# Optimization experiments

Measured on AMD Instinct MI355X. Metric: run time of the kernel, lower is better.

Reference implementation:

```python
import jax, jax.numpy as jnp
import numpy as np

V, D, B, L = 10000, 300, 64, 128
CF = 5.0   # concentrator_factor
EPS = 1e-8  # torch cosine_similarity eps


def setup_inputs() -> dict:
    key = jax.random.key(0)
    ks = jax.random.split(key, 7)
    concepts_list = jax.random.randint(ks[0], (B, L), 0, V)
    concepts_length = jax.random.randint(ks[1], (B,), 0, L + 1)
    embed_w = jax.random.normal(ks[2], (V, D), jnp.float32)
    concept_w = jax.random.normal(ks[3], (V, D), jnp.float32)
    em = jax.random.uniform(ks[4], (V, V), jnp.float32)
    # init_params normalization: row-max minus col-min, per row
    rng = (em.max(axis=1) - em.min(axis=0))[:, None]
    edge_matrix = em / (rng + (rng == 0).astype(em.dtype))
    affectiveness = jax.random.uniform(ks[5], (V,), jnp.float32)
    lam = jax.random.uniform(ks[6], (V,), jnp.float32)
    return {
        "concepts_list": concepts_list,
        "concepts_length": concepts_length,
        "embed_w": embed_w,
        "concept_w": concept_w,
        "edge_matrix": edge_matrix,
        "affectiveness": affectiveness,
        "lam": lam,
    }


def reference(concepts_list, concepts_length, embed_w, concept_w, edge_matrix, affectiveness, lam):
    b, l = concepts_list.shape
    mask = (jnp.arange(l)[None, :] < concepts_length[:, None]).astype(embed_w.dtype)  # [B,L]
    denom = jnp.maximum(concepts_length, 1).astype(embed_w.dtype)[:, None]            # [B,1]

    # context representation: ragged per-sample mean, then mean over batch
    ce = embed_w[concepts_list]                                  # [B,L,D]
    per_sample = (ce * mask[:, :, None]).sum(axis=1) / denom     # [B,D] (zeros for empty)
    context = per_sample.mean(axis=0)                            # [D]

    # |cosine similarity| of context vs every concept embedding row
    cn = jnp.linalg.norm(context)
    rn = jnp.linalg.norm(concept_w, axis=1)                      # [V]
    cos = jnp.abs((concept_w @ context) / jnp.maximum(cn * rn, EPS))  # [V]

    em = edge_matrix[concepts_list]                              # [B,L,V]
    rel = em * cos
    aff = (em > 0).astype(em.dtype) * affectiveness
    weights = lam * rel + (1.0 - lam) * aff                      # [B,L,V]
    probs = jax.nn.softmax(weights * CF, axis=2)                 # [B,L,V]
    ce2 = jnp.einsum('blv,vd->bld', probs, concept_w)            # [B,L,D]

    out = (ce2 * mask[:, :, None]).sum(axis=1) / denom           # [B,D] (zeros for empty)
    return out
```

## Files before the change

kernel.cpp:

```cpp
#include <hip/hip_runtime.h>
#include <math.h>

#define NV 10000
#define ND 300
#define NB 64
#define NL 128
#define CFv 5.0f
#define EPSV 1e-8f

#define WS_CTX   0
#define WS_CN    300
#define WS_CNT   301
#define WS_A     320
#define WS_B     10320
#define WS_ROWS  20320
#define WS_S     28512
#define WS_WTG   36704

#define KR    128
#define WTGLD 10112
#define NKR   79
#define GMG   6
#define NTI   19
#define MT    32
#define SOB   16

typedef __attribute__((ext_vector_type(8))) __bf16 bf16x8;
typedef __attribute__((ext_vector_type(4))) float f32x4;

static __device__ __forceinline__ unsigned short f2bf(float x) {
  union { float f; unsigned u; } v; v.f = x;
  unsigned r = v.u + 0x7fffu + ((v.u >> 16) & 1u);
  return (unsigned short)(r >> 16);
}

__global__ __launch_bounds__(256) void k_init(float* __restrict__ out, float* __restrict__ wsf) {
  int g = blockIdx.x * 256 + threadIdx.x;
  if (g < NB * ND) out[g] = 0.f;
  if (g < 302) wsf[g] = 0.f;
}

#define CSL 4
__global__ __launch_bounds__(320) void k_context(const int* __restrict__ clist,
                                                 const int* __restrict__ clen,
                                                 const float* __restrict__ embed,
                                                 float* __restrict__ wsf) {
  __shared__ int kl[NL];
  int b = blockIdx.x / CSL, sl = blockIdx.x % CSL;
  int d = threadIdx.x;
  int len = clen[b];
  if (d < NL) kl[d] = clist[b * NL + d];
  __syncthreads();
  if (d >= ND) return;
  float acc = 0.f;
  for (int l = sl; l < len; l += CSL)
    acc += embed[(long)kl[l] * ND + d];
  float dn = (float)(len > 0 ? len : 1);
  atomicAdd(&wsf[WS_CTX + d], acc * (1.0f / NB) / dn);
}

__global__ __launch_bounds__(320) void k_cn(float* __restrict__ wsf) {
  __shared__ float red[5];
  int t = threadIdx.x;
  float x = (t < ND) ? wsf[WS_CTX + t] : 0.f;
  float s = x * x;
  #pragma unroll
  for (int o = 32; o; o >>= 1) s += __shfl_xor(s, o);
  if ((t & 63) == 0) red[t >> 6] = s;
  __syncthreads();
  if (t == 0) {
    float tot = 0.f;
    #pragma unroll
    for (int i = 0; i < 5; ++i) tot += red[i];
    wsf[WS_CN] = sqrtf(tot);
  }
}

__global__ __launch_bounds__(256) void k_cos(const float* __restrict__ cw,
                                             const float* __restrict__ lam,
                                             const float* __restrict__ aff,
                                             float* __restrict__ wsf) {
  int wid = threadIdx.x >> 6, lane = threadIdx.x & 63;
  int v = blockIdx.x * 4 + wid;
  const float* row = cw + (long)v * ND;
  float dot = 0.f, rn2 = 0.f;
  for (int d = lane; d < ND; d += 64) {
    float w = row[d], c = wsf[WS_CTX + d];
    dot += w * c;
    rn2 += w * w;
  }
  #pragma unroll
  for (int o = 32; o; o >>= 1) { dot += __shfl_xor(dot, o); rn2 += __shfl_xor(rn2, o); }
  if (lane == 0) {
    float cn = wsf[WS_CN];
    float cosv = fabsf(dot) / fmaxf(cn * sqrtf(rn2), EPSV);
    float lv = lam[v];
    wsf[WS_A + v] = CFv * lv * cosv;
    wsf[WS_B + v] = CFv * (1.f - lv) * aff[v];
  }
}

__global__ __launch_bounds__(256) void k_wt(const float* __restrict__ cw, float* __restrict__ wsf) {
  __shared__ unsigned short T[304][68];
  int tid = threadIdx.x;
  int v0 = blockIdx.x * 64;
  for (int q = tid; q < 304 * 68 / 2; q += 256) ((unsigned*)&T[0][0])[q] = 0u;
  __syncthreads();
  const float4* cw4 = (const float4*)cw;
  for (int q = tid; q < 64 * 75; q += 256) {
    int r = q / 75, p = q - r * 75;
    int v = v0 + r;
    if (v < NV) {
      float4 w = cw4[(long)v * 75 + p];
      T[4 * p + 0][r] = f2bf(w.x);
      T[4 * p + 1][r] = f2bf(w.y);
      T[4 * p + 2][r] = f2bf(w.z);
      T[4 * p + 3][r] = f2bf(w.w);
    }
  }
  __syncthreads();
  unsigned short* wtg = (unsigned short*)(wsf + WS_WTG);
  for (int q = tid; q < 304 * 16; q += 256) {
    int n = q >> 4, rp = q & 15;
    *(ushort4*)&wtg[(long)n * WTGLD + v0 + 4 * rp] = *(const ushort4*)&T[n][4 * rp];
  }
}

__global__ __launch_bounds__(256) void k_compact(const int* __restrict__ clen, int* __restrict__ wsi) {
  __shared__ int cum[NB + 1];
  int tid = threadIdx.x;
  if (tid == 0) {
    int c = 0;
    for (int b = 0; b < NB; ++b) {
      cum[b] = c;
      int ln = clen[b]; if (ln < 0) ln = 0; if (ln > NL) ln = NL;
      c += ln;
    }
    cum[NB] = c;
    wsi[WS_CNT] = c;
  }
  __syncthreads();
  for (int t = tid; t < NB * NL; t += 256) {
    int b = t >> 7, l = t & 127;
    int len = cum[b + 1] - cum[b];
    if (l < len) wsi[WS_ROWS + cum[b] + l] = t;
  }
}

__global__ __launch_bounds__(256) void k_srow(const int* __restrict__ clist,
                                              const float* __restrict__ edge,
                                              float* __restrict__ wsf) {
  const int* wsi = (const int*)wsf;
  int wid = threadIdx.x >> 6, lane = threadIdx.x & 63;
  int pos = blockIdx.x * 4 + wid;
  int count = wsi[WS_CNT];
  if (pos >= count) return;
  int row = wsi[WS_ROWS + pos];
  const float4* e4 = (const float4*)(edge + (long)clist[row] * NV);
  const float4* A4 = (const float4*)(wsf + WS_A);
  const float4* B4 = (const float4*)(wsf + WS_B);
  float sp = 0.f;
  for (int v = lane; v < NV / 4; v += 64) {
    float4 em = e4[v], a = A4[v], b = B4[v];
    sp += __expf(fmaf(a.x, em.x, (em.x > 0.f) ? b.x : 0.f));
    sp += __expf(fmaf(a.y, em.y, (em.y > 0.f) ? b.y : 0.f));
    sp += __expf(fmaf(a.z, em.z, (em.z > 0.f) ? b.z : 0.f));
    sp += __expf(fmaf(a.w, em.w, (em.w > 0.f) ? b.w : 0.f));
  }
  #pragma unroll
  for (int o = 32; o; o >>= 1) sp += __shfl_xor(sp, o);
  if (lane == 0) wsf[WS_S + pos] = sp;
}

__global__ __launch_bounds__(512, 4) void k_main(const int* __restrict__ clist,
                                                 const int* __restrict__ clen,
                                                 const float* __restrict__ edge,
                                                 const float* __restrict__ wsf,
                                                 float* __restrict__ out) {
  __shared__ unsigned short ebuf[2][MT * KR];
  __shared__ float cls[2][KR];
  __shared__ float sout[SOB][304];
  __shared__ int   rb_s[2][MT];
  __shared__ float scl_s[2][MT];

  const int* wsi = (const int*)wsf;
  const unsigned short* wtg = (const unsigned short*)(wsf + WS_WTG);
  int tid = threadIdx.x;
  int count = wsi[WS_CNT];
  int Mtiles = (count + MT - 1) / MT;
  int kr = blockIdx.x / GMG, g = blockIdx.x % GMG;
  int v0 = kr * KR;
  int klen = NV - v0; if (klen > KR) klen = KR;
  int nch = (klen + 31) >> 5;
  int tpg = (Mtiles + GMG - 1) / GMG;
  int mt0 = g * tpg;
  int mt1 = min(mt0 + tpg, Mtiles);

  int b0 = 0;
  {
    int r0c = mt0 * MT;
    if (r0c < count) b0 = wsi[WS_ROWS + r0c] >> 7;
  }

  for (int q = tid; q < 2 * KR; q += 512) {
    int a = q >> 7, k = q & (KR - 1);
    float val = 0.f;
    if (v0 + k < NV) val = wsf[(a ? WS_B : WS_A) + v0 + k];
    cls[a][k] = val;
  }
  for (int q = tid; q < SOB * 304; q += 512) ((float*)sout)[q] = 0.f;

  int wv = tid >> 6, lane = tid & 63;
  int q4 = lane >> 4, l15 = lane & 15;
  int nt0 = (wv * NTI) >> 3, nt1 = ((wv + 1) * NTI) >> 3;

  bf16x8 bfrag[3][4] = {};
  #pragma unroll
  for (int j = 0; j < 3; ++j)
    #pragma unroll
    for (int c5 = 0; c5 < 4; ++c5)
      if (nt0 + j < nt1 && c5 < nch) {
        int n = (nt0 + j) * 16 + l15;
        bfrag[j][c5] = *(const bf16x8*)(const void*)&wtg[(long)n * WTGLD + v0 + c5 * 32 + q4 * 8];
      }

  __syncthreads();

  float4 eld[2];
  int    vld[2];
  int    m_row; float m_scl;

  auto stage_load = [&](int mtx, bool valid) {
    int r0 = mtx * MT;
    #pragma unroll
    for (int j = 0; j < 2; ++j) {
      vld[j] = 0;
      int q = tid + j * 512;
      int rm = q >> 5, k = (q & 31) * 4;
      int pos = r0 + rm;
      if (valid && pos < count && k < klen) {
        int rowid = wsi[WS_ROWS + pos];
        eld[j] = *(const float4*)(edge + (long)clist[rowid] * NV + v0 + k);
        vld[j] = 1;
      }
    }
    m_row = -1; m_scl = 0.f;
    if (tid < MT) {
      int pos = r0 + tid;
      if (valid && pos < count) {
        int rowid = wsi[WS_ROWS + pos];
        float S = wsf[WS_S + pos];
        int ln = clen[rowid >> 7];
        m_row = rowid;
        m_scl = 1.0f / (S * (float)(ln > 0 ? ln : 1));
      }
    }
  };

  auto stage_write = [&](int nb) {
    char* eb = (char*)&ebuf[nb][0];
    #pragma unroll
    for (int j = 0; j < 2; ++j) {
      int q = tid + j * 512;
      int rm = q >> 5, k = (q & 31) * 4;
      ushort4 ev = make_ushort4(0, 0, 0, 0);
      if (vld[j]) {
        float4 a = *(const float4*)&cls[0][k];
        float4 b = *(const float4*)&cls[1][k];
        float4 em = eld[j];
        ev.x = f2bf(__expf(fmaf(a.x, em.x, (em.x > 0.f) ? b.x : 0.f)));
        ev.y = f2bf(__expf(fmaf(a.y, em.y, (em.y > 0.f) ? b.y : 0.f)));
        ev.z = f2bf(__expf(fmaf(a.z, em.z, (em.z > 0.f) ? b.z : 0.f)));
        ev.w = f2bf(__expf(fmaf(a.w, em.w, (em.w > 0.f) ? b.w : 0.f)));
      }
      int off = (rm << 8) + (k << 1);
      off ^= (rm & 7) << 4;
      *(ushort4*)(eb + off) = ev;
    }
    if (tid < MT) { rb_s[nb][tid] = m_row; scl_s[nb][tid] = m_scl; }
  };

  int curb = -1;
  float rs0 = 0.f, rs1 = 0.f, rs2 = 0.f;
  auto emit = [&](int b, float s0, float s1, float s2) {
    if (b < 0) return;
    #pragma unroll
    for (int j = 0; j < 3; ++j) {
      if (nt0 + j < nt1) {
        int n = (nt0 + j) * 16 + l15;
        if (n < ND) {
          float v = (j == 0) ? s0 : (j == 1) ? s1 : s2;
          int rel = b - b0;
          if (rel >= 0 && rel < SOB) atomicAdd(&sout[rel][n], v);
          else atomicAdd(&out[b * ND + n], v);
        }
      }
    }
  };

  if (mt0 < mt1) {
    stage_load(mt0, true);
    stage_write(0);
    __syncthreads();

    int cb = 0;
    for (int mt = mt0; mt < mt1; ++mt) {
      stage_load(mt + 1, mt + 1 < mt1);

      f32x4 acc[2][3] = {};
      const char* eb = (const char*)&ebuf[cb][0];
      #pragma unroll
      for (int c5 = 0; c5 < 4; ++c5) {
        if (c5 < nch) {
          int kb2 = (c5 * 32 + q4 * 8) << 1;
          int off0 = ((l15 << 8) + kb2) ^ ((l15 & 7) << 4);
          int off1 = (((16 + l15) << 8) + kb2) ^ ((l15 & 7) << 4);
          bf16x8 a0 = *(const bf16x8*)(const void*)(eb + off0);
          bf16x8 a1 = *(const bf16x8*)(const void*)(eb + off1);
          #pragma unroll
          for (int j = 0; j < 3; ++j) {
            if (nt0 + j < nt1) {
              acc[0][j] = __builtin_amdgcn_mfma_f32_16x16x32_bf16(a0, bfrag[j][c5], acc[0][j], 0, 0, 0);
              acc[1][j] = __builtin_amdgcn_mfma_f32_16x16x32_bf16(a1, bfrag[j][c5], acc[1][j], 0, 0, 0);
            }
          }
        }
      }

      stage_write(cb ^ 1);

      #pragma unroll
      for (int ms = 0; ms < 2; ++ms)
        #pragma unroll
        for (int r = 0; r < 4; ++r) {
          int m = ms * 16 + q4 * 4 + r;
          int row = rb_s[cb][m];
          if (row >= 0) {
            int b = row >> 7;
            float sc = scl_s[cb][m];
            if (b != curb) {
              emit(curb, rs0, rs1, rs2);
              curb = b; rs0 = rs1 = rs2 = 0.f;
            }
            rs0 += acc[ms][0][r] * sc;
            rs1 += acc[ms][1][r] * sc;
            rs2 += acc[ms][2][r] * sc;
          }
        }

      __syncthreads();
      cb ^= 1;
    }
    emit(curb, rs0, rs1, rs2);
  }
  __syncthreads();

  for (int q = tid; q < SOB * 304; q += 512) {
    int s = q / 304, n = q - s * 304;
    float v = sout[s][n];
    if (n < ND && v != 0.f) {
      int b = b0 + s;
      if (b < NB) atomicAdd(&out[b * ND + n], v);
    }
  }
}

extern "C" void kernel_launch(void* const* d_in, const int* in_sizes, int n_in,
                              void* d_out, int out_size, void* d_ws, size_t ws_size,
                              hipStream_t stream) {
  const int*   clist = (const int*)d_in[0];
  const int*   clen  = (const int*)d_in[1];
  const float* embed = (const float*)d_in[2];
  const float* cw    = (const float*)d_in[3];
  const float* edge  = (const float*)d_in[4];
  const float* aff   = (const float*)d_in[5];
  const float* lam   = (const float*)d_in[6];
  float* out = (float*)d_out;
  float* wsf = (float*)d_ws;
  int*   wsi = (int*)d_ws;

  hipLaunchKernelGGL(k_init,    dim3(77),          dim3(256), 0, stream, out, wsf);
  hipLaunchKernelGGL(k_context, dim3(NB * CSL),    dim3(320), 0, stream, clist, clen, embed, wsf);
  hipLaunchKernelGGL(k_cn,      dim3(1),           dim3(320), 0, stream, wsf);
  hipLaunchKernelGGL(k_cos,     dim3(NV / 4),      dim3(256), 0, stream, cw, lam, aff, wsf);
  hipLaunchKernelGGL(k_wt,      dim3(WTGLD / 64),  dim3(256), 0, stream, cw, wsf);
  hipLaunchKernelGGL(k_compact, dim3(1),           dim3(256), 0, stream, clen, wsi);
  hipLaunchKernelGGL(k_srow,    dim3(NB * NL / 4), dim3(256), 0, stream, clist, edge, wsf);
  hipLaunchKernelGGL(k_main,    dim3(NKR * GMG),   dim3(512), 0, stream,
                     clist, clen, edge, wsf, out);
}
```

Baseline: 180.7 us.

## Deepen main-loop prefetch to two tiles and parallelize row compaction with wave scan

The main loop now holds two register sets of staged edge loads, so global loads for tile mt+2 are issued while tile mt is computed, giving a two-tile prefetch distance instead of one. The loop is manually unrolled by two with named A/B buffers, which avoids dynamic indexing into register arrays. Separately, the compaction kernel replaces its serial prefix sum with a 64-lane shuffle scan and spreads the row scatter across 32 blocks. Keeping extra in-flight registers raises register pressure and could reduce occupancy.

```diff
diff --git a/kernel.cpp b/kernel.cpp
--- a/kernel.cpp
+++ b/kernel.cpp
@@ -129,22 +129,23 @@
 __global__ __launch_bounds__(256) void k_compact(const int* __restrict__ clen, int* __restrict__ wsi) {
   __shared__ int cum[NB + 1];
   int tid = threadIdx.x;
-  if (tid == 0) {
-    int c = 0;
-    for (int b = 0; b < NB; ++b) {
-      cum[b] = c;
-      int ln = clen[b]; if (ln < 0) ln = 0; if (ln > NL) ln = NL;
-      c += ln;
-    }
-    cum[NB] = c;
-    wsi[WS_CNT] = c;
-  }
-  __syncthreads();
-  for (int t = tid; t < NB * NL; t += 256) {
-    int b = t >> 7, l = t & 127;
-    int len = cum[b + 1] - cum[b];
-    if (l < len) wsi[WS_ROWS + cum[b] + l] = t;
-  }
+  if (tid < 64) {
+    int ln = clen[tid]; ln = min(max(ln, 0), NL);
+    int s = ln;
+    #pragma unroll
+    for (int o = 1; o < 64; o <<= 1) {
+      int t = __shfl_up(s, o);
+      if (tid >= o) s += t;
+    }
+    cum[tid + 1] = s;
+    if (tid == 0) cum[0] = 0;
+    if (tid == 63) wsi[WS_CNT] = s;
+  }
+  __syncthreads();
+  int t = blockIdx.x * 256 + tid;
+  int b = t >> 7, l = t & 127;
+  int len = cum[b + 1] - cum[b];
+  if (l < len) wsi[WS_ROWS + cum[b] + l] = t;
 }
 
 __global__ __launch_bounds__(256) void k_srow(const int* __restrict__ clist,
@@ -226,11 +227,13 @@
 
   __syncthreads();
 
-  float4 eld[2];
-  int    vld[2];
-  int    m_row; float m_scl;
-
-  auto stage_load = [&](int mtx, bool valid) {
+  float4 eldA[2], eldB[2];
+  int    vldA[2], vldB[2];
+  int    m_rowA = -1, m_rowB = -1;
+  float  m_sclA = 0.f, m_sclB = 0.f;
+
+  auto stage_load = [&](int mtx, bool valid, float4 (&eld)[2], int (&vld)[2],
+                        int& m_row, float& m_scl) {
     int r0 = mtx * MT;
     #pragma unroll
     for (int j = 0; j < 2; ++j) {
@@ -257,7 +260,8 @@
     }
   };
 
-  auto stage_write = [&](int nb) {
+  auto stage_write = [&](int nb, const float4 (&eld)[2], const int (&vld)[2],
+                         int m_row, float m_scl) {
     char* eb = (char*)&ebuf[nb][0];
     #pragma unroll
     for (int j = 0; j < 2; ++j) {
@@ -280,6 +284,27 @@
     if (tid < MT) { rb_s[nb][tid] = m_row; scl_s[nb][tid] = m_scl; }
   };
 
+  auto do_mfma = [&](int nb, f32x4 (&acc)[2][3]) {
+    const char* eb = (const char*)&ebuf[nb][0];
+    #pragma unroll
+    for (int c5 = 0; c5 < 4; ++c5) {
+      if (c5 < nch) {
+        int kb2 = (c5 * 32 + q4 * 8) << 1;
+        int off0 = ((l15 << 8) + kb2) ^ ((l15 & 7) << 4);
+        int off1 = (((16 + l15) << 8) + kb2) ^ ((l15 & 7) << 4);
+        bf16x8 a0 = *(const bf16x8*)(const void*)(eb + off0);
+        bf16x8 a1 = *(const bf16x8*)(const void*)(eb + off1);
+        #pragma unroll
+        for (int j = 0; j < 3; ++j) {
+          if (nt0 + j < nt1) {
+            acc[0][j] = __builtin_amdgcn_mfma_f32_16x16x32_bf16(a0, bfrag[j][c5], acc[0][j], 0, 0, 0);
+            acc[1][j] = __builtin_amdgcn_mfma_f32_16x16x32_bf16(a1, bfrag[j][c5], acc[1][j], 0, 0, 0);
+          }
+        }
+      }
+    }
+  };
+
   int curb = -1;
   float rs0 = 0.f, rs1 = 0.f, rs2 = 0.f;
   auto emit = [&](int b, float s0, float s1, float s2) {
@@ -298,58 +323,48 @@
     }
   };
 
+  auto fold = [&](const f32x4 (&acc)[2][3], int nb) {
+    #pragma unroll
+    for (int ms = 0; ms < 2; ++ms)
+      #pragma unroll
+      for (int r = 0; r < 4; ++r) {
+        int m = ms * 16 + q4 * 4 + r;
+        int row = rb_s[nb][m];
+        if (row >= 0) {
+          int b = row >> 7;
+          float sc = scl_s[nb][m];
+          if (b != curb) {
+            emit(curb, rs0, rs1, rs2);
+            curb = b; rs0 = rs1 = rs2 = 0.f;
+          }
+          rs0 += acc[ms][0][r] * sc;
+          rs1 += acc[ms][1][r] * sc;
+          rs2 += acc[ms][2][r] * sc;
+        }
+      }
+  };
+
   if (mt0 < mt1) {
-    stage_load(mt0, true);
-    stage_write(0);
+    stage_load(mt0, true, eldA, vldA, m_rowA, m_sclA);
+    stage_write(0, eldA, vldA, m_rowA, m_sclA);
+    stage_load(mt0 + 1, mt0 + 1 < mt1, eldB, vldB, m_rowB, m_sclB);
     __syncthreads();
 
-    int cb = 0;
-    for (int mt = mt0; mt < mt1; ++mt) {
-      stage_load(mt + 1, mt + 1 < mt1);
-
-      f32x4 acc[2][3] = {};
-      const char* eb = (const char*)&ebuf[cb][0];
-      #pragma unroll
-      for (int c5 = 0; c5 < 4; ++c5) {
-        if (c5 < nch) {
-          int kb2 = (c5 * 32 + q4 * 8) << 1;
-          int off0 = ((l15 << 8) + kb2) ^ ((l15 & 7) << 4);
-          int off1 = (((16 + l15) << 8) + kb2) ^ ((l15 & 7) << 4);
-          bf16x8 a0 = *(const bf16x8*)(const void*)(eb + off0);
-          bf16x8 a1 = *(const bf16x8*)(const void*)(eb + off1);
-          #pragma unroll
-          for (int j = 0; j < 3; ++j) {
-            if (nt0 + j < nt1) {
-              acc[0][j] = __builtin_amdgcn_mfma_f32_16x16x32_bf16(a0, bfrag[j][c5], acc[0][j], 0, 0, 0);
-              acc[1][j] = __builtin_amdgcn_mfma_f32_16x16x32_bf16(a1, bfrag[j][c5], acc[1][j], 0, 0, 0);
-            }
-          }
-        }
-      }
-
-      stage_write(cb ^ 1);
-
-      #pragma unroll
-      for (int ms = 0; ms < 2; ++ms)
-        #pragma unroll
-        for (int r = 0; r < 4; ++r) {
-          int m = ms * 16 + q4 * 4 + r;
-          int row = rb_s[cb][m];
-          if (row >= 0) {
-            int b = row >> 7;
-            float sc = scl_s[cb][m];
-            if (b != curb) {
-              emit(curb, rs0, rs1, rs2);
-              curb = b; rs0 = rs1 = rs2 = 0.f;
-            }
-            rs0 += acc[ms][0][r] * sc;
-            rs1 += acc[ms][1][r] * sc;
-            rs2 += acc[ms][2][r] * sc;
-          }
-        }
-
+    for (int mt = mt0; mt < mt1; mt += 2) {
+      stage_load(mt + 2, mt + 2 < mt1, eldA, vldA, m_rowA, m_sclA);
+      f32x4 acc0[2][3] = {};
+      do_mfma(0, acc0);
+      stage_write(1, eldB, vldB, m_rowB, m_sclB);
+      fold(acc0, 0);
       __syncthreads();
-      cb ^= 1;
+      if (mt + 1 < mt1) {
+        stage_load(mt + 3, mt + 3 < mt1, eldB, vldB, m_rowB, m_sclB);
+        f32x4 acc1[2][3] = {};
+        do_mfma(1, acc1);
+        stage_write(0, eldA, vldA, m_rowA, m_sclA);
+        fold(acc1, 1);
+        __syncthreads();
+      }
     }
     emit(curb, rs0, rs1, rs2);
   }
@@ -384,7 +399,7 @@
   hipLaunchKernelGGL(k_cn,      dim3(1),           dim3(320), 0, stream, wsf);
   hipLaunchKernelGGL(k_cos,     dim3(NV / 4),      dim3(256), 0, stream, cw, lam, aff, wsf);
   hipLaunchKernelGGL(k_wt,      dim3(WTGLD / 64),  dim3(256), 0, stream, cw, wsf);
-  hipLaunchKernelGGL(k_compact, dim3(1),           dim3(256), 0, stream, clen, wsi);
+  hipLaunchKernelGGL(k_compact, dim3(32),          dim3(256), 0, stream, clen, wsi);
   hipLaunchKernelGGL(k_srow,    dim3(NB * NL / 4), dim3(256), 0, stream, clist, edge, wsf);
   hipLaunchKernelGGL(k_main,    dim3(NKR * GMG),   dim3(512), 0, stream,
                      clist, clen, edge, wsf, out);
```

Measured after the change: 394.0 us. 118% more time.

## Materialize bf16 exp-weights in row-sum pass and stream them into MFMA kernel

Applied to the files above, without the earlier changes.

The row-sum kernel now also writes the exponentiated, bf16-rounded edge weights for every compacted row into a padded workspace matrix and stores the final per-row scale. The main MFMA kernel reads these bf16 tiles directly from global memory instead of reloading fp32 edge rows, recomputing exp, and staging through double-buffered LDS. This removes duplicate exp work and the second fp32 edge read, at the cost of a large extra workspace write/read and loss of the LDS pipeline and its coalescing/swizzle.

```diff
diff --git a/kernel.cpp b/kernel.cpp
--- a/kernel.cpp
+++ b/kernel.cpp
@@ -16,14 +16,19 @@
 #define WS_ROWS  20320
 #define WS_S     28512
 #define WS_WTG   36704
+#define WS_E     1573760
 
 #define KR    128
 #define WTGLD 10112
+#define ELD   10112
+#define NV4   2500
+#define NV4P  2528
 #define NKR   79
 #define GMG   6
 #define NTI   19
 #define MT    32
 #define SOB   16
+#define TPM   1376
 
 typedef __attribute__((ext_vector_type(8))) __bf16 bf16x8;
 typedef __attribute__((ext_vector_type(4))) float f32x4;
@@ -148,43 +153,56 @@
 }
 
 __global__ __launch_bounds__(256) void k_srow(const int* __restrict__ clist,
+                                              const int* __restrict__ clen,
                                               const float* __restrict__ edge,
                                               float* __restrict__ wsf) {
   const int* wsi = (const int*)wsf;
   int wid = threadIdx.x >> 6, lane = threadIdx.x & 63;
   int pos = blockIdx.x * 4 + wid;
   int count = wsi[WS_CNT];
-  if (pos >= count) return;
+  int countR = (count + 31) & ~31;
+  if (pos >= countR) return;
+  ushort4* Erow = (ushort4*)((unsigned short*)(wsf + WS_E) + (long)pos * ELD);
+  if (pos >= count) {
+    ushort4 z = make_ushort4(0, 0, 0, 0);
+    for (int v = lane; v < NV4P; v += 64) Erow[v] = z;
+    return;
+  }
   int row = wsi[WS_ROWS + pos];
   const float4* e4 = (const float4*)(edge + (long)clist[row] * NV);
   const float4* A4 = (const float4*)(wsf + WS_A);
   const float4* B4 = (const float4*)(wsf + WS_B);
   float sp = 0.f;
-  for (int v = lane; v < NV / 4; v += 64) {
-    float4 em = e4[v], a = A4[v], b = B4[v];
-    sp += __expf(fmaf(a.x, em.x, (em.x > 0.f) ? b.x : 0.f));
-    sp += __expf(fmaf(a.y, em.y, (em.y > 0.f) ? b.y : 0.f));
-    sp += __expf(fmaf(a.z, em.z, (em.z > 0.f) ? b.z : 0.f));
-    sp += __expf(fmaf(a.w, em.w, (em.w > 0.f) ? b.w : 0.f));
+  for (int v = lane; v < NV4P; v += 64) {
+    ushort4 ev = make_ushort4(0, 0, 0, 0);
+    if (v < NV4) {
+      float4 em = e4[v], a = A4[v], b = B4[v];
+      float e0 = __expf(fmaf(a.x, em.x, (em.x > 0.f) ? b.x : 0.f));
+      float e1 = __expf(fmaf(a.y, em.y, (em.y > 0.f) ? b.y : 0.f));
+      float e2 = __expf(fmaf(a.z, em.z, (em.z > 0.f) ? b.z : 0.f));
+      float e3 = __expf(fmaf(a.w, em.w, (em.w > 0.f) ? b.w : 0.f));
+      sp += e0 + e1 + e2 + e3;
+      ev.x = f2bf(e0); ev.y = f2bf(e1); ev.z = f2bf(e2); ev.w = f2bf(e3);
+    }
+    Erow[v] = ev;
   }
   #pragma unroll
   for (int o = 32; o; o >>= 1) sp += __shfl_xor(sp, o);
-  if (lane == 0) wsf[WS_S + pos] = sp;
-}
-
-__global__ __launch_bounds__(512, 4) void k_main(const int* __restrict__ clist,
-                                                 const int* __restrict__ clen,
-                                                 const float* __restrict__ edge,
-                                                 const float* __restrict__ wsf,
+  if (lane == 0) {
+    int ln = clen[row >> 7];
+    wsf[WS_S + pos] = 1.0f / (sp * (float)(ln > 0 ? ln : 1));
+  }
+}
+
+__global__ __launch_bounds__(512, 4) void k_main(const float* __restrict__ wsf,
                                                  float* __restrict__ out) {
-  __shared__ unsigned short ebuf[2][MT * KR];
-  __shared__ float cls[2][KR];
   __shared__ float sout[SOB][304];
-  __shared__ int   rb_s[2][MT];
-  __shared__ float scl_s[2][MT];
+  __shared__ int   rbv[TPM];
+  __shared__ float sclv[TPM];
 
   const int* wsi = (const int*)wsf;
   const unsigned short* wtg = (const unsigned short*)(wsf + WS_WTG);
+  const unsigned short* E = (const unsigned short*)(wsf + WS_E);
   int tid = threadIdx.x;
   int count = wsi[WS_CNT];
   int Mtiles = (count + MT - 1) / MT;
@@ -202,14 +220,6 @@
     if (r0c < count) b0 = wsi[WS_ROWS + r0c] >> 7;
   }
 
-  for (int q = tid; q < 2 * KR; q += 512) {
-    int a = q >> 7, k = q & (KR - 1);
-    float val = 0.f;
-    if (v0 + k < NV) val = wsf[(a ? WS_B : WS_A) + v0 + k];
-    cls[a][k] = val;
-  }
-  for (int q = tid; q < SOB * 304; q += 512) ((float*)sout)[q] = 0.f;
-
   int wv = tid >> 6, lane = tid & 63;
   int q4 = lane >> 4, l15 = lane & 15;
   int nt0 = (wv * NTI) >> 3, nt1 = ((wv + 1) * NTI) >> 3;
@@ -224,72 +234,29 @@
         bfrag[j][c5] = *(const bf16x8*)(const void*)&wtg[(long)n * WTGLD + v0 + c5 * 32 + q4 * 8];
       }
 
-  __syncthreads();
-
-  float4 eld[2];
-  int    vld[2];
-  int    m_row; float m_scl;
-
-  auto stage_load = [&](int mtx, bool valid) {
-    int r0 = mtx * MT;
-    #pragma unroll
-    for (int j = 0; j < 2; ++j) {
-      vld[j] = 0;
-      int q = tid + j * 512;
-      int rm = q >> 5, k = (q & 31) * 4;
-      int pos = r0 + rm;
-      if (valid && pos < count && k < klen) {
-        int rowid = wsi[WS_ROWS + pos];
-        eld[j] = *(const float4*)(edge + (long)clist[rowid] * NV + v0 + k);
-        vld[j] = 1;
-      }
-    }
-    m_row = -1; m_scl = 0.f;
-    if (tid < MT) {
-      int pos = r0 + tid;
-      if (valid && pos < count) {
-        int rowid = wsi[WS_ROWS + pos];
-        float S = wsf[WS_S + pos];
-        int ln = clen[rowid >> 7];
-        m_row = rowid;
-        m_scl = 1.0f / (S * (float)(ln > 0 ? ln : 1));
-      }
-    }
-  };
-
-  auto stage_write = [&](int nb) {
-    char* eb = (char*)&ebuf[nb][0];
-    #pragma unroll
-    for (int j = 0; j < 2; ++j) {
-      int q = tid + j * 512;
-      int rm = q >> 5, k = (q & 31) * 4;
-      ushort4 ev = make_ushort4(0, 0, 0, 0);
-      if (vld[j]) {
-        float4 a = *(const float4*)&cls[0][k];
-        float4 b = *(const float4*)&cls[1][k];
-        float4 em = eld[j];
-        ev.x = f2bf(__expf(fmaf(a.x, em.x, (em.x > 0.f) ? b.x : 0.f)));
-        ev.y = f2bf(__expf(fmaf(a.y, em.y, (em.y > 0.f) ? b.y : 0.f)));
-        ev.z = f2bf(__expf(fmaf(a.z, em.z, (em.z > 0.f) ? b.z : 0.f)));
-        ev.w = f2bf(__expf(fmaf(a.w, em.w, (em.w > 0.f) ? b.w : 0.f)));
-      }
-      int off = (rm << 8) + (k << 1);
-      off ^= (rm & 7) << 4;
-      *(ushort4*)(eb + off) = ev;
-    }
-    if (tid < MT) { rb_s[nb][tid] = m_row; scl_s[nb][tid] = m_scl; }
-  };
+  for (int q = tid; q < SOB * 304; q += 512) ((float*)sout)[q] = 0.f;
+  int nloc = (mt1 > mt0) ? (mt1 - mt0) * MT : 0;
+  for (int i = tid; i < TPM; i += 512) {
+    int rv = -1; float sc = 0.f;
+    int pos = mt0 * MT + i;
+    if (i < nloc && pos < count) {
+      rv = wsi[WS_ROWS + pos];
+      sc = wsf[WS_S + pos];
+    }
+    rbv[i] = rv; sclv[i] = sc;
+  }
+  __syncthreads();
 
   int curb = -1;
   float rs0 = 0.f, rs1 = 0.f, rs2 = 0.f;
-  auto emit = [&](int b, float s0, float s1, float s2) {
+  auto emit = [&](int b) {
     if (b < 0) return;
     #pragma unroll
     for (int j = 0; j < 3; ++j) {
       if (nt0 + j < nt1) {
         int n = (nt0 + j) * 16 + l15;
         if (n < ND) {
-          float v = (j == 0) ? s0 : (j == 1) ? s1 : s2;
+          float v = (j == 0) ? rs0 : (j == 1) ? rs1 : rs2;
           int rel = b - b0;
           if (rel >= 0 && rel < SOB) atomicAdd(&sout[rel][n], v);
           else atomicAdd(&out[b * ND + n], v);
@@ -298,61 +265,47 @@
     }
   };
 
-  if (mt0 < mt1) {
-    stage_load(mt0, true);
-    stage_write(0);
-    __syncthreads();
-
-    int cb = 0;
-    for (int mt = mt0; mt < mt1; ++mt) {
-      stage_load(mt + 1, mt + 1 < mt1);
-
-      f32x4 acc[2][3] = {};
-      const char* eb = (const char*)&ebuf[cb][0];
-      #pragma unroll
-      for (int c5 = 0; c5 < 4; ++c5) {
-        if (c5 < nch) {
-          int kb2 = (c5 * 32 + q4 * 8) << 1;
-          int off0 = ((l15 << 8) + kb2) ^ ((l15 & 7) << 4);
-          int off1 = (((16 + l15) << 8) + kb2) ^ ((l15 & 7) << 4);
-          bf16x8 a0 = *(const bf16x8*)(const void*)(eb + off0);
-          bf16x8 a1 = *(const bf16x8*)(const void*)(eb + off1);
-          #pragma unroll
-          for (int j = 0; j < 3; ++j) {
-            if (nt0 + j < nt1) {
-              acc[0][j] = __builtin_amdgcn_mfma_f32_16x16x32_bf16(a0, bfrag[j][c5], acc[0][j], 0, 0, 0);
-              acc[1][j] = __builtin_amdgcn_mfma_f32_16x16x32_bf16(a1, bfrag[j][c5], acc[1][j], 0, 0, 0);
-            }
+  for (int mt = mt0; mt < mt1; ++mt) {
+    long eb0 = (long)(mt * MT + l15) * ELD + v0;
+    long eb1 = (long)(mt * MT + 16 + l15) * ELD + v0;
+    f32x4 acc[2][3] = {};
+    #pragma unroll
+    for (int c5 = 0; c5 < 4; ++c5) {
+      if (c5 < nch) {
+        int ko = c5 * 32 + q4 * 8;
+        bf16x8 a0 = *(const bf16x8*)(const void*)&E[eb0 + ko];
+        bf16x8 a1 = *(const bf16x8*)(const void*)&E[eb1 + ko];
+        #pragma unroll
+        for (int j = 0; j < 3; ++j) {
+          if (nt0 + j < nt1) {
+            acc[0][j] = __builtin_amdgcn_mfma_f32_16x16x32_bf16(a0, bfrag[j][c5], acc[0][j], 0, 0, 0);
+            acc[1][j] = __builtin_amdgcn_mfma_f32_16x16x32_bf16(a1, bfrag[j][c5], acc[1][j], 0, 0, 0);
           }
         }
       }
-
-      stage_write(cb ^ 1);
-
+    }
+
+    #pragma unroll
+    for (int ms = 0; ms < 2; ++ms)
       #pragma unroll
-      for (int ms = 0; ms < 2; ++ms)
-        #pragma unroll
-        for (int r = 0; r < 4; ++r) {
-          int m = ms * 16 + q4 * 4 + r;
-          int row = rb_s[cb][m];
-          if (row >= 0) {
-            int b = row >> 7;
-            float sc = scl_s[cb][m];
-            if (b != curb) {
-              emit(curb, rs0, rs1, rs2);
-              curb = b; rs0 = rs1 = rs2 = 0.f;
-            }
-            rs0 += acc[ms][0][r] * sc;
-            rs1 += acc[ms][1][r] * sc;
-            rs2 += acc[ms][2][r] * sc;
+      for (int r = 0; r < 4; ++r) {
+        int m = ms * 16 + q4 * 4 + r;
+        int i = (mt - mt0) * MT + m;
+        int row = rbv[i];
+        if (row >= 0) {
+          int b = row >> 7;
+          float sc = sclv[i];
+          if (b != curb) {
+            emit(curb);
+            curb = b; rs0 = rs1 = rs2 = 0.f;
           }
+          rs0 += acc[ms][0][r] * sc;
+          rs1 += acc[ms][1][r] * sc;
+          rs2 += acc[ms][2][r] * sc;
         }
-
-      __syncthreads();
-      cb ^= 1;
-    }
-    emit(curb, rs0, rs1, rs2);
-  }
+      }
+  }
+  emit(curb);
   __syncthreads();
 
   for (int q = tid; q < SOB * 304; q += 512) {
@@ -385,7 +338,6 @@
   hipLaunchKernelGGL(k_cos,     dim3(NV / 4),      dim3(256), 0, stream, cw, lam, aff, wsf);
   hipLaunchKernelGGL(k_wt,      dim3(WTGLD / 64),  dim3(256), 0, stream, cw, wsf);
   hipLaunchKernelGGL(k_compact, dim3(1),           dim3(256), 0, stream, clen, wsi);
-  hipLaunchKernelGGL(k_srow,    dim3(NB * NL / 4), dim3(256), 0, stream, clist, edge, wsf);
-  hipLaunchKernelGGL(k_main,    dim3(NKR * GMG),   dim3(512), 0, stream,
-                     clist, clen, edge, wsf, out);
-}
+  hipLaunchKernelGGL(k_srow,    dim3(NB * NL / 4), dim3(256), 0, stream, clist, clen, edge, wsf);
+  hipLaunchKernelGGL(k_main,    dim3(NKR * GMG),   dim3(512), 0, stream, wsf, out);
+}
```

Measured after the change: 194.0 us. +7.4%, slower.
